# Kernel tuning notes

Measured on AMD Instinct MI355X. Metric: run time of the kernel, lower is better.

The kernel has to match this reference:

```python
import jax, jax.numpy as jnp
import numpy as np

B, T, D_IN, H, C = 4096, 20, 300, 512, 10


def setup_inputs() -> dict:
    key = jax.random.key(0)
    ks = jax.random.split(key, 12)
    s = lambda fan_in, fan_out: float(np.sqrt(6.0 / (fan_in + fan_out)))  # xavier uniform bound
    u = lambda k, shape, b: jax.random.uniform(k, shape, jnp.float32, -b, b)
    return {
        "x": jax.random.normal(ks[0], (B, T, D_IN), jnp.float32),
        "W_emb": u(ks[1], (D_IN, H), s(D_IN, H)),
        "b_emb": jnp.zeros((H,), jnp.float32),
        "wx0": u(ks[2], (H, H), s(H, H)),
        "wh0": u(ks[3], (H, H), s(H, H)),
        "b0": jnp.zeros((H,), jnp.float32),
        "wx1": u(ks[4], (H, H), s(H, H)),
        "wh1": u(ks[5], (H, H), s(H, H)),
        "b1": jnp.zeros((H,), jnp.float32),
        "wx2": u(ks[6], (H, H), s(H, H)),
        "wh2": u(ks[7], (H, H), s(H, H)),
        "b2": jnp.zeros((H,), jnp.float32),
        "W_fc": u(ks[8], (H, C), s(H, C)),
        "b_fc": jnp.zeros((C,), jnp.float32),
    }


def reference(x, W_emb, b_emb, wx0, wh0, b0, wx1, wh1, b1, wx2, wh2, b2, W_fc, b_fc):
    # embedding_layer applied to all timesteps: [B,T,300] -> [B,T,512]
    emb = jnp.einsum("btd,dh->bth", x, W_emb) + b_emb
    h0 = jnp.zeros((x.shape[0], wx0.shape[1]), x.dtype)
    init = (h0, h0, h0)

    def step(carry, v_t):  # v_t: [B,H]
        h0, h1, h2 = carry
        h0 = jnp.tanh(v_t @ wx0 + h0 @ wh0 + b0)
        h1 = jnp.tanh(h0 @ wx1 + h1 @ wh1 + b1)
        h2 = jnp.tanh(h1 @ wx2 + h2 @ wh2 + b2)
        return (h0, h1, h2), None

    (h0, h1, h2), _ = jax.lax.scan(step, init, jnp.swapaxes(emb, 0, 1))  # scan over T
    return h2 @ W_fc + b_fc  # [B, C]
```

## Files before the change

### kernel.cpp

```cpp
#include <hip/hip_runtime.h>

typedef _Float16 f16;
typedef _Float16 f16x8 __attribute__((ext_vector_type(8)));
typedef float floatx4 __attribute__((ext_vector_type(4)));

__device__ __forceinline__ float ftanh(float x) {
  float ax = __builtin_fabsf(x);
  float e  = __expf(-2.0f * ax);
  float t  = (1.0f - e) * __builtin_amdgcn_rcpf(1.0f + e);
  return x < 0.0f ? -t : t;
}

__device__ __forceinline__ void gll16(const f16* g, f16* l) {
  __builtin_amdgcn_global_load_lds(
      (const __attribute__((address_space(1))) void*)g,
      (__attribute__((address_space(3))) void*)l, 16, 0, 0);
}

template<int FJ>
__device__ __forceinline__ void tile_gemm(
    const f16* __restrict__ A0, int ldA0,
    const f16* __restrict__ A1, int ldA1,
    int K, const f16* __restrict__ WT, int ldW,
    const float* __restrict__ bias,
    f16* __restrict__ outp, int bm, int bn, f16* sm)
{
  const int tid  = threadIdx.x;
  const int w    = tid >> 6;
  const int lane = tid & 63;
  const int lm   = lane & 15;
  const int quad = lane >> 4;
  const int wm   = (w >> 1) * 64;
  const int wn   = (w & 1) * (FJ * 16);
  const int srow8 = lane >> 3;
  const int scol  = ((lane & 7) ^ srow8) * 8;
  const int lmx   = lane & 7;
  constexpr int SB = 8192 + FJ * 2048;

  floatx4 acc[4][FJ];
  #pragma unroll
  for (int i = 0; i < 4; ++i)
    #pragma unroll
    for (int j = 0; j < FJ; ++j)
      acc[i][j] = (floatx4){0.f, 0.f, 0.f, 0.f};

  auto stage = [&](int buf, int k0) {
    const f16* Asrc = (k0 < 512) ? (A0 + k0) : (A1 + (k0 - 512));
    const int  ld   = (k0 < 512) ? ldA0 : ldA1;
    f16* As0 = sm + buf * SB;
    f16* Ws0 = As0 + 8192;
    #pragma unroll
    for (int i = 0; i < 4; ++i) {
      int r = (w * 4 + i) * 8 + srow8;
      gll16(Asrc + (size_t)(bm + r) * ld + scol, As0 + (w * 4 + i) * 512);
    }
    #pragma unroll
    for (int i = 0; i < FJ; ++i) {
      int r = (w * FJ + i) * 8 + srow8;
      gll16(WT + (size_t)(bn + r) * ldW + k0 + scol, Ws0 + (w * FJ + i) * 512);
    }
  };

  const int NS = K >> 6;
  stage(0, 0);
  __syncthreads();
  for (int s = 0; s < NS; ++s) {
    if (s + 1 < NS) stage((s + 1) & 1, (s + 1) << 6);
    const f16* As0 = sm + (s & 1) * SB;
    const f16* Ws0 = As0 + 8192;
    #pragma unroll
    for (int kk = 0; kk < 64; kk += 32) {
      const int sw = (((kk >> 3) + quad) ^ lmx) << 3;
      f16x8 a[4], bfr[FJ];
      #pragma unroll
      for (int fi = 0; fi < 4; ++fi)
        a[fi] = *(const f16x8*)&As0[(size_t)(wm + fi * 16 + lm) * 64 + sw];
      #pragma unroll
      for (int fj = 0; fj < FJ; ++fj)
        bfr[fj] = *(const f16x8*)&Ws0[(size_t)(wn + fj * 16 + lm) * 64 + sw];
      __builtin_amdgcn_s_setprio(1);
      #pragma unroll
      for (int fi = 0; fi < 4; ++fi)
        #pragma unroll
        for (int fj = 0; fj < FJ; ++fj)
          acc[fi][fj] = __builtin_amdgcn_mfma_f32_16x16x32_f16(a[fi], bfr[fj], acc[fi][fj], 0, 0, 0);
      __builtin_amdgcn_s_setprio(0);
    }
    __syncthreads();
  }

  constexpr int ES = FJ * 32 + 8;
  #pragma unroll
  for (int fi = 0; fi < 4; ++fi)
    #pragma unroll
    for (int fj = 0; fj < FJ; ++fj) {
      int col = wn + fj * 16 + lm;
      #pragma unroll
      for (int r = 0; r < 4; ++r) {
        int row = wm + fi * 16 + quad * 4 + r;
        sm[row * ES + col] = (f16)acc[fi][fj][r];
      }
    }
  __syncthreads();
  constexpr int TPR = (FJ * 32) / 8;
  constexpr int RPP = 256 / TPR;
  #pragma unroll
  for (int p = 0; p < 128 / RPP; ++p) {
    int row = p * RPP + tid / TPR;
    int c8  = (tid % TPR) * 8;
    f16x8 ve = *(const f16x8*)&sm[row * ES + c8];
    floatx4 bv0 = *(const floatx4*)&bias[bn + c8];
    floatx4 bv1 = *(const floatx4*)&bias[bn + c8 + 4];
    union { f16 e[8]; f16x8 v; } o;
    #pragma unroll
    for (int j = 0; j < 4; ++j) o.e[j]     = (f16)ftanh((float)ve[j]     + bv0[j]);
    #pragma unroll
    for (int j = 0; j < 4; ++j) o.e[4 + j] = (f16)ftanh((float)ve[4 + j] + bv1[j]);
    *(f16x8*)(outp + (size_t)(bm + row) * 512 + bn + c8) = o.v;
  }
}

__global__ __launch_bounds__(256, 2)
void rnn_step(int wv, const f16* __restrict__ xh,
              const f16* __restrict__ W0T, const f16* __restrict__ W1T,
              const f16* __restrict__ W2T,
              const float* __restrict__ bcomb, const float* __restrict__ b1,
              const float* __restrict__ b2,
              const f16* __restrict__ H0c, f16* __restrict__ H0n,
              const f16* __restrict__ H1c, f16* __restrict__ H1n,
              const f16* __restrict__ H2c, f16* __restrict__ H2n)
{
  __shared__ f16 sm[32768];
  const int b   = blockIdx.x;
  const int xcd = b & 7;
  const int r   = b >> 3;

  if (r < 32) {
    if (wv > 19) return;
    const int slab = xcd * 4 + (r & 3);
    const int bn   = (r >> 2) * 64;
    if (wv == 0)
      tile_gemm<2>(xh, 6400, xh, 6400, 320, W0T + 512, 832, bcomb,
                   H0n, slab * 128, bn, sm);
    else
      tile_gemm<2>(H0c, 512, xh + (size_t)wv * 320, 6400, 832, W0T, 832, bcomb,
                   H0n, slab * 128, bn, sm);
  } else if (r < 48) {
    if (wv < 1 || wv > 20) return;
    const int rr   = r - 32;
    const int slab = xcd * 4 + (rr & 3);
    const int bn   = (rr >> 2) * 128;
    if (wv == 1)
      tile_gemm<4>(H0c, 512, H0c, 512, 512, W1T, 1024, b1, H1n, slab * 128, bn, sm);
    else
      tile_gemm<4>(H0c, 512, H1c, 512, 1024, W1T, 1024, b1, H1n, slab * 128, bn, sm);
  } else {
    if (wv < 2) return;
    const int rr   = r - 48;
    const int slab = xcd * 4 + (rr & 3);
    const int bn   = (rr >> 2) * 128;
    if (wv == 2)
      tile_gemm<4>(H1c, 512, H1c, 512, 512, W2T, 1024, b2, H2n, slab * 128, bn, sm);
    else
      tile_gemm<4>(H1c, 512, H2c, 512, 1024, W2T, 1024, b2, H2n, slab * 128, bn, sm);
  }
}

#define P_XH  1600
#define P_WCE 2240
#define P_BC  2248
#define P_Z   2888

__global__ __launch_bounds__(256)
void prep_all(const float* __restrict__ x,
              const float* __restrict__ W_emb, const float* __restrict__ b_emb,
              const float* __restrict__ wx0, const float* __restrict__ wh0,
              const float* __restrict__ b0,
              const float* __restrict__ wx1, const float* __restrict__ wh1,
              const float* __restrict__ wx2, const float* __restrict__ wh2,
              f16* __restrict__ xh, f16* __restrict__ W0T,
              f16* __restrict__ W1T, f16* __restrict__ W2T,
              float* __restrict__ bcomb)
{
  __shared__ float smem[16384];
  const int b   = blockIdx.x;
  const int tid = threadIdx.x;
  const floatx4 z4 = {0.f, 0.f, 0.f, 0.f};

  if (b < P_XH) {
    const int NTH = P_XH * 256;
    const int g = b * 256 + tid;
    floatx4 va[8], vb[8];
    int rw[8], cc[8];
    #pragma unroll
    for (int s = 0; s < 8; ++s) {
      int U = g + s * NTH;
      int row = U / 40;
      int c   = (U - row * 40) * 8;
      rw[s] = row; cc[s] = c;
      const float* src = x + (size_t)row * 300 + c;
      va[s] = (c + 4 <= 300) ? *(const floatx4*)src : z4;
      vb[s] = (c + 8 <= 300) ? *(const floatx4*)(src + 4) : z4;
    }
    #pragma unroll
    for (int s = 0; s < 8; ++s) {
      union { f16 e[8]; f16x8 v; } t;
      #pragma unroll
      for (int j = 0; j < 4; ++j) { t.e[j] = (f16)va[s][j]; t.e[4 + j] = (f16)vb[s][j]; }
      *(f16x8*)(xh + (size_t)rw[s] * 320 + cc[s]) = t.v;
    }
  } else if (b < P_WCE) {
    float* wes = smem;
    float* wxs = smem + 8192;
    const int bb = b - P_XH;
    const int kt = bb >> 5, nt = bb & 31;
    const int k0 = kt * 16, n0 = nt * 16;
    const int rr = tid >> 4, cc = tid & 15;
    {
      const int k = k0 + rr;
      #pragma unroll
      for (int q = 0; q < 8; ++q) {
        floatx4 v = (k < 300) ? *(const floatx4*)&W_emb[(size_t)k * 512 + cc * 32 + q * 4] : z4;
        *(floatx4*)&wes[rr * 512 + cc * 32 + q * 4] = v;
      }
    }
    #pragma unroll 4
    for (int jj = 0; jj < 32; ++jj) {
      int j = rr * 32 + jj;
      wxs[j * 16 + cc] = wx0[(size_t)j * 512 + n0 + cc];
    }
    __syncthreads();
    float s = 0.f;
    #pragma unroll 8
    for (int j = 0; j < 512; ++j)
      s = __builtin_fmaf(wes[rr * 512 + j], wxs[j * 16 + cc], s);
    W0T[(size_t)(n0 + cc) * 832 + 512 + k0 + rr] = (f16)s;
  } else if (b < P_BC) {
    float* red = smem;
    int n     = (b - P_WCE) * 64 + (tid & 63);
    int chunk = tid >> 6;
    float s = 0.f;
    const float* be = b_emb + chunk * 128;
    const float* wx = wx0 + (size_t)(chunk * 128) * 512 + n;
    #pragma unroll 4
    for (int j = 0; j < 128; ++j)
      s = __builtin_fmaf(be[j], wx[(size_t)j * 512], s);
    red[tid] = s;
    __syncthreads();
    if (chunk == 0)
      bcomb[n] = b0[n] + red[tid] + red[tid + 64] + red[tid + 128] + red[tid + 192];
  } else {
    int id = (b - P_BC) * 256 + tid;
    if (id < 32768) {
      int n = id & 511, k8 = id >> 9;
      union { f16 e[8]; f16x8 v; } t;
      #pragma unroll
      for (int j = 0; j < 8; ++j) t.e[j] = (f16)wh0[(size_t)(k8 * 8 + j) * 512 + n];
      *(f16x8*)&W0T[(size_t)n * 832 + k8 * 8] = t.v;
    } else if (id < 98304) {
      int i2 = id - 32768;
      int n = i2 & 511, k8 = i2 >> 9;
      union { f16 e[8]; f16x8 v; } t;
      const float* src = (k8 < 64) ? (wx1 + (size_t)(k8 * 8) * 512 + n)
                                   : (wh1 + (size_t)((k8 - 64) * 8) * 512 + n);
      #pragma unroll
      for (int j = 0; j < 8; ++j) t.e[j] = (f16)src[(size_t)j * 512];
      *(f16x8*)&W1T[(size_t)n * 1024 + k8 * 8] = t.v;
    } else {
      int i2 = id - 98304;
      int n = i2 & 511, k8 = i2 >> 9;
      union { f16 e[8]; f16x8 v; } t;
      const float* src = (k8 < 64) ? (wx2 + (size_t)(k8 * 8) * 512 + n)
                                   : (wh2 + (size_t)((k8 - 64) * 8) * 512 + n);
      #pragma unroll
      for (int j = 0; j < 8; ++j) t.e[j] = (f16)src[(size_t)j * 512];
      *(f16x8*)&W2T[(size_t)n * 1024 + k8 * 8] = t.v;
    }
  }
}

__global__ void fc_kernel(const f16* __restrict__ h2,
                          const float* __restrict__ Wfc, const float* __restrict__ bfc,
                          float* __restrict__ out)
{
  __shared__ float wf[5120];
  __shared__ float bf[16];
  const int tid = threadIdx.x;
  for (int i = tid; i < 5120; i += 256) wf[i] = Wfc[i];
  if (tid < 10) bf[tid] = bfc[tid];
  __syncthreads();
  int id = blockIdx.x * 256 + tid;
  int row = id / 10;
  int c = id - row * 10;
  float s = bf[c];
  const f16* hr = h2 + (size_t)row * 512;
  for (int k8 = 0; k8 < 64; ++k8) {
    f16x8 h8 = *(const f16x8*)(hr + k8 * 8);
    #pragma unroll
    for (int j = 0; j < 8; ++j)
      s = __builtin_fmaf((float)h8[j], wf[(k8 * 8 + j) * 10 + c], s);
  }
  out[id] = s;
}

extern "C" void kernel_launch(void* const* d_in, const int* in_sizes, int n_in,
                              void* d_out, int out_size, void* d_ws, size_t ws_size,
                              hipStream_t stream)
{
  (void)in_sizes; (void)n_in; (void)out_size; (void)ws_size;
  const float* x     = (const float*)d_in[0];
  const float* W_emb = (const float*)d_in[1];
  const float* b_emb = (const float*)d_in[2];
  const float* wx0   = (const float*)d_in[3];
  const float* wh0   = (const float*)d_in[4];
  const float* b0    = (const float*)d_in[5];
  const float* wx1   = (const float*)d_in[6];
  const float* wh1   = (const float*)d_in[7];
  const float* b1    = (const float*)d_in[8];
  const float* wx2   = (const float*)d_in[9];
  const float* wh2   = (const float*)d_in[10];
  const float* b2    = (const float*)d_in[11];
  const float* W_fc  = (const float*)d_in[12];
  const float* b_fc  = (const float*)d_in[13];
  float* out = (float*)d_out;

  char* ws = (char*)d_ws;
  size_t off = 0;
  auto alloc = [&](size_t bytes) -> void* {
    void* p = ws + off;
    off = (off + bytes + 255) & ~(size_t)255;
    return p;
  };
  f16*   xh    = (f16*)alloc((size_t)81920 * 320 * 2);
  f16*   W0T   = (f16*)alloc((size_t)512 * 832 * 2);
  f16*   W1T   = (f16*)alloc((size_t)512 * 1024 * 2);
  f16*   W2T   = (f16*)alloc((size_t)512 * 1024 * 2);
  float* bcomb = (float*)alloc(512 * 4);
  f16*   H0a   = (f16*)alloc((size_t)4096 * 512 * 2);
  f16*   H0b   = (f16*)alloc((size_t)4096 * 512 * 2);
  f16*   H1a   = (f16*)alloc((size_t)4096 * 512 * 2);
  f16*   H1b   = (f16*)alloc((size_t)4096 * 512 * 2);
  f16*   H2a   = (f16*)alloc((size_t)4096 * 512 * 2);
  f16*   H2b   = (f16*)alloc((size_t)4096 * 512 * 2);

  prep_all<<<P_Z, 256, 0, stream>>>(x, W_emb, b_emb, wx0, wh0, b0,
                                    wx1, wh1, wx2, wh2,
                                    xh, W0T, W1T, W2T, bcomb);

  for (int wv = 0; wv < 22; ++wv) {
    const int cur = wv & 1;
    f16* H0c = cur ? H0b : H0a;  f16* H0n = cur ? H0a : H0b;
    f16* H1c = cur ? H1b : H1a;  f16* H1n = cur ? H1a : H1b;
    f16* H2c = cur ? H2b : H2a;  f16* H2n = cur ? H2a : H2b;
    rnn_step<<<512, 256, 0, stream>>>(wv, xh, W0T, W1T, W2T, bcomb, b1, b2,
                                      H0c, H0n, H1c, H1n, H2c, H2n);
  }

  fc_kernel<<<160, 256, 0, stream>>>(H2a, W_fc, b_fc, out);
}
```

Baseline: 566.4 us.

## Move recurrent weight transposes into idle blocks of the first wavefront step

The fp32-to-fp16 transposes of wh0, wx1/wh1 and wx2/wh2 move out of the prep kernel. They now run in the otherwise idle layer-1/2 blocks of the first rnn_step launch, overlapping with layer-0 work. The prep kernel is split into prep_x and prep_w to shorten the serial prologue. Risk: the wv==0 layer-0 tiles use only the W_emb-fused part of W0T (prepared earlier), so this stays correct, but the layer-1 path at wv==0 is now gated only by the new branch.

```diff
diff --git a/kernel.cpp b/kernel.cpp
--- a/kernel.cpp
+++ b/kernel.cpp
@@ -122,10 +122,13 @@
 
 __global__ __launch_bounds__(256, 2)
 void rnn_step(int wv, const f16* __restrict__ xh,
-              const f16* __restrict__ W0T, const f16* __restrict__ W1T,
-              const f16* __restrict__ W2T,
+              f16* __restrict__ W0T, f16* __restrict__ W1T,
+              f16* __restrict__ W2T,
               const float* __restrict__ bcomb, const float* __restrict__ b1,
               const float* __restrict__ b2,
+              const float* __restrict__ wh0, const float* __restrict__ wx1,
+              const float* __restrict__ wh1, const float* __restrict__ wx2,
+              const float* __restrict__ wh2,
               const f16* __restrict__ H0c, f16* __restrict__ H0n,
               const f16* __restrict__ H1c, f16* __restrict__ H1n,
               const f16* __restrict__ H2c, f16* __restrict__ H2n)
@@ -145,8 +148,38 @@
     else
       tile_gemm<2>(H0c, 512, xh + (size_t)wv * 320, 6400, 832, W0T, 832, bcomb,
                    H0n, slab * 128, bn, sm);
+  } else if (wv == 0) {
+    const int fb = b - 256;
+    for (int c = threadIdx.x; c < 640; c += 256) {
+      int id = fb * 640 + c;
+      if (id < 32768) {
+        int n = id & 511, k8 = id >> 9;
+        union { f16 e[8]; f16x8 v; } t;
+        #pragma unroll
+        for (int j = 0; j < 8; ++j) t.e[j] = (f16)wh0[(size_t)(k8 * 8 + j) * 512 + n];
+        *(f16x8*)&W0T[(size_t)n * 832 + k8 * 8] = t.v;
+      } else if (id < 98304) {
+        int i2 = id - 32768;
+        int n = i2 & 511, k8 = i2 >> 9;
+        union { f16 e[8]; f16x8 v; } t;
+        const float* src = (k8 < 64) ? (wx1 + (size_t)(k8 * 8) * 512 + n)
+                                     : (wh1 + (size_t)((k8 - 64) * 8) * 512 + n);
+        #pragma unroll
+        for (int j = 0; j < 8; ++j) t.e[j] = (f16)src[(size_t)j * 512];
+        *(f16x8*)&W1T[(size_t)n * 1024 + k8 * 8] = t.v;
+      } else {
+        int i2 = id - 98304;
+        int n = i2 & 511, k8 = i2 >> 9;
+        union { f16 e[8]; f16x8 v; } t;
+        const float* src = (k8 < 64) ? (wx2 + (size_t)(k8 * 8) * 512 + n)
+                                     : (wh2 + (size_t)((k8 - 64) * 8) * 512 + n);
+        #pragma unroll
+        for (int j = 0; j < 8; ++j) t.e[j] = (f16)src[(size_t)j * 512];
+        *(f16x8*)&W2T[(size_t)n * 1024 + k8 * 8] = t.v;
+      }
+    }
   } else if (r < 48) {
-    if (wv < 1 || wv > 20) return;
+    if (wv > 20) return;
     const int rr   = r - 32;
     const int slab = xcd * 4 + (rr & 3);
     const int bn   = (rr >> 2) * 128;
@@ -166,54 +199,52 @@
   }
 }
 
-#define P_XH  1600
-#define P_WCE 2240
-#define P_BC  2248
-#define P_Z   2888
+#define PX_N 1600
 
 __global__ __launch_bounds__(256)
-void prep_all(const float* __restrict__ x,
-              const float* __restrict__ W_emb, const float* __restrict__ b_emb,
-              const float* __restrict__ wx0, const float* __restrict__ wh0,
-              const float* __restrict__ b0,
-              const float* __restrict__ wx1, const float* __restrict__ wh1,
-              const float* __restrict__ wx2, const float* __restrict__ wh2,
-              f16* __restrict__ xh, f16* __restrict__ W0T,
-              f16* __restrict__ W1T, f16* __restrict__ W2T,
-              float* __restrict__ bcomb)
+void prep_x(const float* __restrict__ x, f16* __restrict__ xh)
+{
+  const int NTH = PX_N * 256;
+  const int g = blockIdx.x * 256 + threadIdx.x;
+  floatx4 va[8], vb[8];
+  int rw[8], cc[8];
+  const floatx4 z4 = {0.f, 0.f, 0.f, 0.f};
+  #pragma unroll
+  for (int s = 0; s < 8; ++s) {
+    int U = g + s * NTH;
+    int row = U / 40;
+    int c   = (U - row * 40) * 8;
+    rw[s] = row; cc[s] = c;
+    const float* src = x + (size_t)row * 300 + c;
+    va[s] = (c + 4 <= 300) ? *(const floatx4*)src : z4;
+    vb[s] = (c + 8 <= 300) ? *(const floatx4*)(src + 4) : z4;
+  }
+  #pragma unroll
+  for (int s = 0; s < 8; ++s) {
+    union { f16 e[8]; f16x8 v; } t;
+    #pragma unroll
+    for (int j = 0; j < 4; ++j) { t.e[j] = (f16)va[s][j]; t.e[4 + j] = (f16)vb[s][j]; }
+    *(f16x8*)(xh + (size_t)rw[s] * 320 + cc[s]) = t.v;
+  }
+}
+
+#define QW_WCE 640
+#define QW_Z   648
+
+__global__ __launch_bounds__(256)
+void prep_w(const float* __restrict__ W_emb, const float* __restrict__ b_emb,
+            const float* __restrict__ wx0, const float* __restrict__ b0,
+            f16* __restrict__ W0T, float* __restrict__ bcomb)
 {
   __shared__ float smem[16384];
   const int b   = blockIdx.x;
   const int tid = threadIdx.x;
   const floatx4 z4 = {0.f, 0.f, 0.f, 0.f};
 
-  if (b < P_XH) {
-    const int NTH = P_XH * 256;
-    const int g = b * 256 + tid;
-    floatx4 va[8], vb[8];
-    int rw[8], cc[8];
-    #pragma unroll
-    for (int s = 0; s < 8; ++s) {
-      int U = g + s * NTH;
-      int row = U / 40;
-      int c   = (U - row * 40) * 8;
-      rw[s] = row; cc[s] = c;
-      const float* src = x + (size_t)row * 300 + c;
-      va[s] = (c + 4 <= 300) ? *(const floatx4*)src : z4;
-      vb[s] = (c + 8 <= 300) ? *(const floatx4*)(src + 4) : z4;
-    }
-    #pragma unroll
-    for (int s = 0; s < 8; ++s) {
-      union { f16 e[8]; f16x8 v; } t;
-      #pragma unroll
-      for (int j = 0; j < 4; ++j) { t.e[j] = (f16)va[s][j]; t.e[4 + j] = (f16)vb[s][j]; }
-      *(f16x8*)(xh + (size_t)rw[s] * 320 + cc[s]) = t.v;
-    }
-  } else if (b < P_WCE) {
+  if (b < QW_WCE) {
     float* wes = smem;
     float* wxs = smem + 8192;
-    const int bb = b - P_XH;
-    const int kt = bb >> 5, nt = bb & 31;
+    const int kt = b >> 5, nt = b & 31;
     const int k0 = kt * 16, n0 = nt * 16;
     const int rr = tid >> 4, cc = tid & 15;
     {
@@ -235,9 +266,9 @@
     for (int j = 0; j < 512; ++j)
       s = __builtin_fmaf(wes[rr * 512 + j], wxs[j * 16 + cc], s);
     W0T[(size_t)(n0 + cc) * 832 + 512 + k0 + rr] = (f16)s;
-  } else if (b < P_BC) {
+  } else {
     float* red = smem;
-    int n     = (b - P_WCE) * 64 + (tid & 63);
+    int n     = (b - QW_WCE) * 64 + (tid & 63);
     int chunk = tid >> 6;
     float s = 0.f;
     const float* be = b_emb + chunk * 128;
@@ -249,33 +280,6 @@
     __syncthreads();
     if (chunk == 0)
       bcomb[n] = b0[n] + red[tid] + red[tid + 64] + red[tid + 128] + red[tid + 192];
-  } else {
-    int id = (b - P_BC) * 256 + tid;
-    if (id < 32768) {
-      int n = id & 511, k8 = id >> 9;
-      union { f16 e[8]; f16x8 v; } t;
-      #pragma unroll
-      for (int j = 0; j < 8; ++j) t.e[j] = (f16)wh0[(size_t)(k8 * 8 + j) * 512 + n];
-      *(f16x8*)&W0T[(size_t)n * 832 + k8 * 8] = t.v;
-    } else if (id < 98304) {
-      int i2 = id - 32768;
-      int n = i2 & 511, k8 = i2 >> 9;
-      union { f16 e[8]; f16x8 v; } t;
-      const float* src = (k8 < 64) ? (wx1 + (size_t)(k8 * 8) * 512 + n)
-                                   : (wh1 + (size_t)((k8 - 64) * 8) * 512 + n);
-      #pragma unroll
-      for (int j = 0; j < 8; ++j) t.e[j] = (f16)src[(size_t)j * 512];
-      *(f16x8*)&W1T[(size_t)n * 1024 + k8 * 8] = t.v;
-    } else {
-      int i2 = id - 98304;
-      int n = i2 & 511, k8 = i2 >> 9;
-      union { f16 e[8]; f16x8 v; } t;
-      const float* src = (k8 < 64) ? (wx2 + (size_t)(k8 * 8) * 512 + n)
-                                   : (wh2 + (size_t)((k8 - 64) * 8) * 512 + n);
-      #pragma unroll
-      for (int j = 0; j < 8; ++j) t.e[j] = (f16)src[(size_t)j * 512];
-      *(f16x8*)&W2T[(size_t)n * 1024 + k8 * 8] = t.v;
-    }
   }
 }
 
@@ -343,9 +347,8 @@
   f16*   H2a   = (f16*)alloc((size_t)4096 * 512 * 2);
   f16*   H2b   = (f16*)alloc((size_t)4096 * 512 * 2);
 
-  prep_all<<<P_Z, 256, 0, stream>>>(x, W_emb, b_emb, wx0, wh0, b0,
-                                    wx1, wh1, wx2, wh2,
-                                    xh, W0T, W1T, W2T, bcomb);
+  prep_x<<<PX_N, 256, 0, stream>>>(x, xh);
+  prep_w<<<QW_Z, 256, 0, stream>>>(W_emb, b_emb, wx0, b0, W0T, bcomb);
 
   for (int wv = 0; wv < 22; ++wv) {
     const int cur = wv & 1;
@@ -353,6 +356,7 @@
     f16* H1c = cur ? H1b : H1a;  f16* H1n = cur ? H1a : H1b;
     f16* H2c = cur ? H2b : H2a;  f16* H2n = cur ? H2a : H2b;
     rnn_step<<<512, 256, 0, stream>>>(wv, xh, W0T, W1T, W2T, bcomb, b1, b2,
+                                      wh0, wx1, wh1, wx2, wh2,
                                       H0c, H0n, H1c, H1n, H2c, H2n);
   }
 
```

After: 590.0 us. +4.2%, slower.
